# Kernel tuning notes

Measured on AMD Instinct MI355X. Metric: run time of the kernel, lower is better.

Reference implementation:

```python
import jax, jax.numpy as jnp
import numpy as np

B, LQ, LK = 4, 4096, 4096
D = 1024          # num_heads * key_dim = 16 * 64
Q_DIM = 1024      # query_dim
K_DIM = 1024      # note: linear_k input dim; here inputs carry d_model features
V_DIM = 1024      # value_dim


def setup_inputs() -> dict:
    key = jax.random.key(0)
    ks = jax.random.split(key, 12)
    s_in = 1.0 / np.sqrt(Q_DIM)
    s_d = 1.0 / np.sqrt(D)
    return {
        "q": jax.random.normal(ks[0], (B, LQ, Q_DIM), jnp.float32),
        "k": jax.random.normal(ks[1], (B, LK, K_DIM), jnp.float32),
        "v": jax.random.normal(ks[2], (B, LK, V_DIM), jnp.float32),
        # Linear weights stored [in, out] so projection is x @ W + b
        "Wq": jax.random.normal(ks[3], (Q_DIM, D), jnp.float32) * s_in,
        "bq": jax.random.normal(ks[4], (D,), jnp.float32) * s_in,
        "Wk": jax.random.normal(ks[5], (K_DIM, D), jnp.float32) * s_in,
        "bk": jax.random.normal(ks[6], (D,), jnp.float32) * s_in,
        "Wv": jax.random.normal(ks[7], (V_DIM, D), jnp.float32) * s_in,
        "bv": jax.random.normal(ks[8], (D,), jnp.float32) * s_in,
        "Wo": jax.random.normal(ks[9], (D, V_DIM), jnp.float32) * s_d,
        "bo": jax.random.normal(ks[10], (V_DIM,), jnp.float32) * s_d,
    }


def reference(q, k, v, Wq, bq, Wk, bk, Wv, bv, Wo, bo):
    # Projections: [B, L, D]
    qp = jax.nn.softmax(q @ Wq + bq, axis=-1)   # softmax over feature dim
    kp = jax.nn.softmax(k @ Wk + bk, axis=-2)   # softmax over sequence dim
    vp = jax.nn.softmax(v @ Wv + bv, axis=-2)   # softmax over sequence dim
    # Dropout is identity in eval mode (module uses dropout_p at train only).
    scores = jnp.einsum("bqd,bkd->bqk", qp, kp)  # [B, LQ, LK]
    ctx = jnp.einsum("bqk,bkd->bqd", scores, vp)  # [B, LQ, D]
    return ctx @ Wo + bo                          # [B, LQ, V_DIM]
```

## Files before the change

kernel.cpp:

```cpp
#include <hip/hip_runtime.h>

typedef float f32x4 __attribute__((ext_vector_type(4)));
typedef long lx2 __attribute__((ext_vector_type(2)));

__device__ __forceinline__ float h2f(unsigned short h) {
  return (float)__builtin_bit_cast(_Float16, h);
}
__device__ __forceinline__ unsigned short f2h(float f) {
  return __builtin_bit_cast(unsigned short, (_Float16)f);
}

#if __has_builtin(__builtin_amdgcn_cvt_pk_fp8_f32)
#define HW_FP8 1
#else
#define HW_FP8 0
#endif

__device__ __forceinline__ unsigned char f2e4_sw(float f) {
  unsigned short h = __builtin_bit_cast(unsigned short, (_Float16)f);
  unsigned s = (h >> 8) & 0x80u;
  unsigned ae = h & 0x7FFFu;
  if (ae >= 0x5F00u) return (unsigned char)(s | 0x7Eu);
  if (ae >= 0x2400u) {
    unsigned t = ae - 0x2000u;
    t = (t + 0x3Fu + ((t >> 7) & 1u)) >> 7;
    return (unsigned char)(s | t);
  }
  float v = (float)__builtin_bit_cast(_Float16, (unsigned short)ae) * 512.0f;
  int n = (int)rintf(v);
  return (unsigned char)(s | (unsigned)n);
}

__device__ __forceinline__ unsigned pk4e4(float a, float b, float c, float d) {
#if HW_FP8
  int lo = __builtin_amdgcn_cvt_pk_fp8_f32(a, b, 0, false);
  return (unsigned)__builtin_amdgcn_cvt_pk_fp8_f32(c, d, lo, true);
#else
  return (unsigned)f2e4_sw(a) | ((unsigned)f2e4_sw(b) << 8) |
         ((unsigned)f2e4_sw(c) << 16) | ((unsigned)f2e4_sw(d) << 24);
#endif
}
__device__ __forceinline__ unsigned pk2e4(float a, float b) {
#if HW_FP8
  return (unsigned)__builtin_amdgcn_cvt_pk_fp8_f32(a, b, 0, false) & 0xFFFFu;
#else
  return (unsigned)f2e4_sw(a) | ((unsigned)f2e4_sw(b) << 8);
#endif
}

__device__ __forceinline__ void gload_lds16(const void* g, void* l) {
  __builtin_amdgcn_global_load_lds(
      (const __attribute__((address_space(1))) void*)g,
      (__attribute__((address_space(3))) void*)l, 16, 0, 0);
}

__global__ __launch_bounds__(512, 4) void proj3(
    const float* __restrict__ A0, const float* __restrict__ A1,
    const float* __restrict__ A2, const unsigned char* __restrict__ WT8b,
    const float* __restrict__ b0, const float* __restrict__ b1,
    const float* __restrict__ b2, unsigned char* __restrict__ C0,
    unsigned char* __restrict__ C1, unsigned char* __restrict__ C2,
    float* __restrict__ s0, float* __restrict__ s1, float* __restrict__ s2)
{
  __shared__ alignas(16) unsigned char smem[49152];
  const int tid  = threadIdx.x;
  const int lane = tid & 63;
  const int wave = tid >> 6;
  const int waveM = wave >> 2;
  const int waveN = wave & 3;

  const int wg = (int)blockIdx.x;
  const int w  = (wg & 7) * 192 + (wg >> 3);
  const int z  = w / 512;
  const int wl = w - z * 512;
  const int x  = wl & 3;
  const int rem = wl >> 2;
  const int y  = rem & 31;
  const int bz = rem >> 5;

  const float* Af = (z == 0) ? A0 : (z == 1) ? A1 : A2;
  const float* bi = (z == 0) ? b0 : (z == 1) ? b1 : b2;
  unsigned char* Cp = (z == 0) ? C0 : (z == 1) ? C1 : C2;
  float* sums = (z == 0) ? s0 : (z == 1) ? s1 : s2;

  const int m0 = y * 128, n0 = x * 256;

  const int srow = tid >> 3;
  const int scol = ((tid * 16) & 127) ^ ((srow & 7) << 4);
  const unsigned char* BpR = WT8b + ((size_t)z << 20)
                             + (size_t)(n0 + srow) * 1024 + scol;
  const float* ApR = Af + (size_t)bz * (4096L * 1024)
                     + (size_t)(m0 + srow) * 1024 + scol;
  const unsigned oA0 = (unsigned)tid * 16;

  int offA[4], offB[4];
  {
    const int q16 = (lane >> 4) << 4;
#pragma unroll
    for (int mi = 0; mi < 4; ++mi) {
      const int r = waveM * 64 + mi * 16 + (lane & 15);
      offA[mi] = r * 128 + (q16 ^ ((r & 7) << 4));
    }
#pragma unroll
    for (int ni = 0; ni < 4; ++ni) {
      const int r = waveN * 64 + ni * 16 + (lane & 15);
      offB[ni] = 16384 + r * 128 + (q16 ^ ((r & 7) << 4));
    }
  }

  f32x4 acc[4][4] = {};

  float4 pa[4], pb[4];
#pragma unroll
  for (int j = 0; j < 4; ++j) {
    pa[j] = *(const float4*)(ApR + j * 4);
    pb[j] = *(const float4*)(ApR + 64 * 1024 + j * 4);
  }

  for (int kt = 0; kt < 8; ++kt) {
    {
      unsigned ua[4], ub[4];
#pragma unroll
      for (int j = 0; j < 4; ++j) {
        ua[j] = pk4e4(pa[j].x, pa[j].y, pa[j].z, pa[j].w);
        ub[j] = pk4e4(pb[j].x, pb[j].y, pb[j].z, pb[j].w);
      }
      *(uint4*)&smem[oA0]        = *(const uint4*)ua;
      *(uint4*)&smem[oA0 + 8192] = *(const uint4*)ub;
      if (kt + 1 < 8) {
        const float* s = ApR + (size_t)(kt + 1) * 128;
#pragma unroll
        for (int j = 0; j < 4; ++j) {
          pa[j] = *(const float4*)(s + j * 4);
          pb[j] = *(const float4*)(s + 64 * 1024 + j * 4);
        }
      }
    }
    const size_t kb = (size_t)kt * 128;
    gload_lds16(BpR + kb,              smem + 16384 + oA0);
    gload_lds16(BpR + 64 * 1024 + kb,  smem + 16384 + oA0 + 8192);
    gload_lds16(BpR + 128 * 1024 + kb, smem + 16384 + oA0 + 16384);
    gload_lds16(BpR + 192 * 1024 + kb, smem + 16384 + oA0 + 24576);
    __syncthreads();
#pragma unroll
    for (int kk = 0; kk < 2; ++kk) {
      const int kx = kk << 6;
      lx2 aF[4], bF[4];
#pragma unroll
      for (int mi = 0; mi < 4; ++mi) aF[mi] = *(const lx2*)&smem[offA[mi] ^ kx];
#pragma unroll
      for (int ni = 0; ni < 4; ++ni) bF[ni] = *(const lx2*)&smem[offB[ni] ^ kx];
#pragma unroll
      for (int h = 0; h < 2; ++h)
#pragma unroll
        for (int mi = 0; mi < 4; ++mi)
#pragma unroll
          for (int ni = 0; ni < 4; ++ni)
            acc[mi][ni] = __builtin_amdgcn_mfma_f32_16x16x32_fp8_fp8(
                aF[mi][h], bF[ni][h], acc[mi][ni], 0, 0, 0);
    }
    __syncthreads();
  }

  const int rb = (lane >> 4) * 4;
  const int cb_ = lane & 15;
  const long sC = 4096L * 1024;

  if (z == 0) {
#pragma unroll
    for (int m = 0; m < 4; ++m) {
      const int row0 = m0 + waveM * 64 + m * 16 + rb;
      float rs0 = 0, rs1 = 0, rs2 = 0, rs3 = 0;
#pragma unroll
      for (int n = 0; n < 4; ++n) {
        const int col = n0 + waveN * 64 + n * 16 + cb_;
        const float badd = bi[col];
        const float e0 = __expf(acc[m][n][0] * 0.125f + badd);
        const float e1 = __expf(acc[m][n][1] * 0.125f + badd);
        const float e2 = __expf(acc[m][n][2] * 0.125f + badd);
        const float e3 = __expf(acc[m][n][3] * 0.125f + badd);
        const unsigned p01 = pk2e4(e0 * 0.0625f, e1 * 0.0625f);
        const unsigned p23 = pk2e4(e2 * 0.0625f, e3 * 0.0625f);
        unsigned char* C8 = Cp + (long)bz * sC;
        C8[(size_t)(row0 + 0) * 1024 + col] = (unsigned char)(p01 & 0xff);
        C8[(size_t)(row0 + 1) * 1024 + col] = (unsigned char)((p01 >> 8) & 0xff);
        C8[(size_t)(row0 + 2) * 1024 + col] = (unsigned char)(p23 & 0xff);
        C8[(size_t)(row0 + 3) * 1024 + col] = (unsigned char)((p23 >> 8) & 0xff);
        rs0 += e0; rs1 += e1; rs2 += e2; rs3 += e3;
      }
#pragma unroll
      for (int off = 1; off <= 8; off <<= 1) {
        rs0 += __shfl_xor(rs0, off);
        rs1 += __shfl_xor(rs1, off);
        rs2 += __shfl_xor(rs2, off);
        rs3 += __shfl_xor(rs3, off);
      }
      if ((lane & 15) == 0) {
        float* s = sums + (size_t)bz * 4096 + row0;
        atomicAdd(s + 0, rs0);
        atomicAdd(s + 1, rs1);
        atomicAdd(s + 2, rs2);
        atomicAdd(s + 3, rs3);
      }
    }
  } else {
    float cs[4] = {0.f, 0.f, 0.f, 0.f};
#pragma unroll
    for (int m = 0; m < 4; ++m) {
      const int row0 = m0 + waveM * 64 + m * 16 + rb;
#pragma unroll
      for (int n = 0; n < 4; ++n) {
        const int col = n0 + waveN * 64 + n * 16 + cb_;
        const float badd = bi[col];
        float ev[4];
        float ls = 0.f;
#pragma unroll
        for (int r = 0; r < 4; ++r) {
          ev[r] = __expf(acc[m][n][r] * 0.125f + badd);
          ls += ev[r];
        }
        cs[n] += ls;
        *(unsigned*)(Cp + (long)bz * sC + ((size_t)col << 12) + row0) =
            pk4e4(ev[0] * 0.0625f, ev[1] * 0.0625f, ev[2] * 0.0625f, ev[3] * 0.0625f);
      }
    }
#pragma unroll
    for (int n = 0; n < 4; ++n) {
      cs[n] += __shfl_xor(cs[n], 16);
      cs[n] += __shfl_xor(cs[n], 32);
    }
    if (lane < 16) {
#pragma unroll
      for (int n = 0; n < 4; ++n) {
        const int col = n0 + waveN * 64 + n * 16 + lane;
        atomicAdd(sums + ((size_t)bz << 10) + col, cs[n]);
      }
    }
  }
}

template <int OUTMODE>
__global__ __launch_bounds__(512, 4) void gemm8(
    const unsigned char* __restrict__ A, const unsigned char* __restrict__ Bt,
    void* __restrict__ Cv, const float* __restrict__ bias,
    const float* __restrict__ sums,
    int N, int K, int ldk, int gx, int gy, int nsplit,
    long sA, long sB, long sC)
{
  __shared__ alignas(16) unsigned char smem[49152];
  const int tid  = threadIdx.x;
  const int lane = tid & 63;
  const int wave = tid >> 6;
  const int waveM = wave >> 2;
  const int waveN = wave & 3;

  const int nwg = (int)gridDim.x;
  const int cpx = nwg >> 3;
  const int wg  = (int)blockIdx.x;
  const int w   = (wg & 7) * cpx + (wg >> 3);
  const int x   = w % gx;
  const int rem = w / gx;
  const int y   = rem % gy;
  const int zt  = rem / gy;
  const int bz  = zt / nsplit;
  const int sp  = zt % nsplit;

  const int m0 = y * 128, n0 = x * 256;
  const size_t ldkB = (size_t)ldk;
  const size_t ldkB64 = ldkB * 64, ldkB128 = ldkB * 128;

  const int srow = tid >> 3;
  const int scol = ((tid * 16) & 127) ^ ((srow & 7) << 4);
  const char* ApR;
  const char* BpR;
  {
    const char* Ab = (const char*)A + (long)bz * sA + (long)sp * K + (size_t)m0 * ldkB;
    const char* Bb = (const char*)Bt + (long)bz * sB + (long)sp * K + (size_t)n0 * ldkB;
    ApR = Ab + (size_t)srow * ldkB + scol;
    BpR = Bb + (size_t)srow * ldkB + scol;
  }
  const unsigned oA0 = (unsigned)tid * 16;

  int offA[4], offB[4];
  {
    const int q16 = (lane >> 4) << 4;
#pragma unroll
    for (int mi = 0; mi < 4; ++mi) {
      const int r = waveM * 64 + mi * 16 + (lane & 15);
      offA[mi] = r * 128 + (q16 ^ ((r & 7) << 4));
    }
#pragma unroll
    for (int ni = 0; ni < 4; ++ni) {
      const int r = waveN * 64 + ni * 16 + (lane & 15);
      offB[ni] = 16384 + r * 128 + (q16 ^ ((r & 7) << 4));
    }
  }

  f32x4 acc[4][4] = {};

  const int nk = K >> 7;
  for (int kt = 0; kt < nk; ++kt) {
    const size_t kb = (size_t)kt * 128;
    gload_lds16(ApR + kb,                     smem + oA0);
    gload_lds16(ApR + ldkB64 + kb,            smem + oA0 + 8192);
    gload_lds16(BpR + kb,                     smem + 16384 + oA0);
    gload_lds16(BpR + ldkB64 + kb,            smem + 16384 + oA0 + 8192);
    gload_lds16(BpR + ldkB128 + kb,           smem + 16384 + oA0 + 16384);
    gload_lds16(BpR + ldkB128 + ldkB64 + kb,  smem + 16384 + oA0 + 24576);
    __syncthreads();
#pragma unroll
    for (int kk = 0; kk < 2; ++kk) {
      const int kx = kk << 6;
      lx2 aF[4], bF[4];
#pragma unroll
      for (int mi = 0; mi < 4; ++mi) aF[mi] = *(const lx2*)&smem[offA[mi] ^ kx];
#pragma unroll
      for (int ni = 0; ni < 4; ++ni) bF[ni] = *(const lx2*)&smem[offB[ni] ^ kx];
#pragma unroll
      for (int h = 0; h < 2; ++h)
#pragma unroll
        for (int mi = 0; mi < 4; ++mi)
#pragma unroll
          for (int ni = 0; ni < 4; ++ni)
            acc[mi][ni] = __builtin_amdgcn_mfma_f32_16x16x32_fp8_fp8(
                aF[mi][h], bF[ni][h], acc[mi][ni], 0, 0, 0);
    }
    __syncthreads();
  }

  const int rb = (lane >> 4) * 4;
  const int cb_ = lane & 15;
  const long zout = (OUTMODE == 2) ? (long)zt : (long)bz;
#pragma unroll
  for (int m = 0; m < 4; ++m) {
    const int row0 = m0 + waveM * 64 + m * 16 + rb;
    float i0 = 0, i1 = 0, i2 = 0, i3 = 0;
    if (OUTMODE == 5) {
      const float4 s4 = *(const float4*)&sums[(size_t)zout * 4096 + row0];
      i0 = 1.0f / (256.0f * s4.x); i1 = 1.0f / (256.0f * s4.y);
      i2 = 1.0f / (256.0f * s4.z); i3 = 1.0f / (256.0f * s4.w);
    }
#pragma unroll
    for (int n = 0; n < 4; ++n) {
      const int col = n0 + waveN * 64 + n * 16 + cb_;
      if (OUTMODE == 2) {
#pragma unroll
        for (int r = 0; r < 4; ++r)
          ((unsigned short*)Cv)[zout * sC + (size_t)(row0 + r) * N + col] = f2h(acc[m][n][r]);
      } else {
        const float badd = bias[col];
        float* C32 = (float*)Cv;
        C32[zout * sC + (size_t)(row0 + 0) * N + col] = acc[m][n][0] * i0 + badd;
        C32[zout * sC + (size_t)(row0 + 1) * N + col] = acc[m][n][1] * i1 + badd;
        C32[zout * sC + (size_t)(row0 + 2) * N + col] = acc[m][n][2] * i2 + badd;
        C32[zout * sC + (size_t)(row0 + 3) * N + col] = acc[m][n][3] * i3 + badd;
      }
    }
  }
}

__global__ __launch_bounds__(256) void w_tr8(
    const float* __restrict__ W0, const float* __restrict__ W1,
    const float* __restrict__ W2, const float* __restrict__ W3,
    unsigned char* __restrict__ WT8b)
{
  __shared__ float tile[64][65];
  const int z = blockIdx.z;
  const float* W = (z == 0) ? W0 : (z == 1) ? W1 : (z == 2) ? W2 : W3;
  unsigned char* WT8 = WT8b + ((size_t)z << 20);
  const int c0 = blockIdx.x * 64;
  const int r0 = blockIdx.y * 64;
  const int tid = threadIdx.x;
  const int r = tid >> 2;
  const int cq = (tid & 3) * 16;
#pragma unroll
  for (int i = 0; i < 4; ++i) {
    const int c = cq + i * 4;
    const float4 v = *(const float4*)&W[(size_t)(r0 + r) * 1024 + c0 + c];
    tile[r][c + 0] = v.x;
    tile[r][c + 1] = v.y;
    tile[r][c + 2] = v.z;
    tile[r][c + 3] = v.w;
  }
  __syncthreads();
  const int c = tid >> 2;
  const int rq = (tid & 3) * 16;
  unsigned u4[4];
#pragma unroll
  for (int j = 0; j < 4; ++j)
    u4[j] = pk4e4(tile[rq + 4 * j + 0][c] * 8.f, tile[rq + 4 * j + 1][c] * 8.f,
                  tile[rq + 4 * j + 2][c] * 8.f, tile[rq + 4 * j + 3][c] * 8.f);
  *(uint4*)(WT8 + (size_t)(c0 + c) * 1024 + r0 + rq) = *(const uint4*)u4;
}

__global__ __launch_bounds__(256) void red4m(
    const unsigned short* __restrict__ P, const float* __restrict__ skr,
    const float* __restrict__ svr, unsigned char* __restrict__ O)
{
  const int i = blockIdx.x * 256 + threadIdx.x;
  const int b = i >> 18;
  const int j = i & 262143;
  const int dk = j >> 8;
  const int dv0 = (j & 255) << 2;
  float s0 = 0, s1 = 0, s2 = 0, s3 = 0;
#pragma unroll
  for (int sl = 0; sl < 4; ++sl) {
    const uint2 u = *(const uint2*)(P + (((long)(b * 4 + sl)) << 20) + ((long)j << 2));
    s0 += h2f(u.x & 0xffff); s1 += h2f(u.x >> 16);
    s2 += h2f(u.y & 0xffff); s3 += h2f(u.y >> 16);
  }
  const float fk = 4194304.0f / skr[(b << 10) + dk];
  const float4 fv = *(const float4*)&svr[(b << 10) + dv0];
  ((unsigned*)O)[i] = pk4e4(s0 * fk / fv.x, s1 * fk / fv.y,
                            s2 * fk / fv.z, s3 * fk / fv.w);
}

__global__ __launch_bounds__(256) void red4g(
    const unsigned short* __restrict__ P, unsigned char* __restrict__ O)
{
  const int i = blockIdx.x * 256 + threadIdx.x;
  const int b = i >> 18;
  const int j = i & 262143;
  float s0 = 0, s1 = 0, s2 = 0, s3 = 0;
#pragma unroll
  for (int sl = 0; sl < 4; ++sl) {
    const uint2 u = *(const uint2*)(P + (((long)(b * 4 + sl)) << 20) + ((long)j << 2));
    s0 += h2f(u.x & 0xffff); s1 += h2f(u.x >> 16);
    s2 += h2f(u.y & 0xffff); s3 += h2f(u.y >> 16);
  }
  ((unsigned*)O)[i] = pk4e4(s0 * 0.03125f, s1 * 0.03125f,
                            s2 * 0.03125f, s3 * 0.03125f);
}

extern "C" void kernel_launch(void* const* d_in, const int* in_sizes, int n_in,
                              void* d_out, int out_size, void* d_ws, size_t ws_size,
                              hipStream_t stream) {
  const float* q  = (const float*)d_in[0];
  const float* k  = (const float*)d_in[1];
  const float* v  = (const float*)d_in[2];
  const float* Wq = (const float*)d_in[3];
  const float* bq = (const float*)d_in[4];
  const float* Wk = (const float*)d_in[5];
  const float* bk = (const float*)d_in[6];
  const float* Wv = (const float*)d_in[7];
  const float* bv = (const float*)d_in[8];
  const float* Wo = (const float*)d_in[9];
  const float* bo = (const float*)d_in[10];
  float* out = (float*)d_out;

  char* p = (char*)d_ws;
  unsigned short* Part = (unsigned short*)p; p += 33554432;
  unsigned char* WT8b = (unsigned char*)p;   p += 4194304;
  unsigned char* Eq8  = (unsigned char*)p;   p += 16777216;
  unsigned char* ETk8 = (unsigned char*)p;   p += 16777216;
  unsigned char* ETv8 = (unsigned char*)p;   p += 16777216;
  unsigned char* Mh8  = (unsigned char*)p;   p += 4194304;
  unsigned char* GT8  = (unsigned char*)p;   p += 4194304;
  float* sqraw = (float*)p; p += 16384 * 4;
  float* skraw = (float*)p; p += 4096 * 4;
  float* svraw = (float*)p; p += 4096 * 4;

  const dim3 blk(256);
  const dim3 blk512(512);
  const long S22 = 4096L * 1024;
  const long S20 = 1024L * 1024;

  hipMemsetAsync(sqraw, 0, (16384 + 4096 + 4096) * sizeof(float), stream);

  w_tr8<<<dim3(16, 16, 4), blk, 0, stream>>>(Wq, Wk, Wv, Wo, WT8b);

  proj3<<<1536, blk512, 0, stream>>>(q, k, v, WT8b, bq, bk, bv,
                                     Eq8, ETk8, ETv8, sqraw, skraw, svraw);

  gemm8<2><<<512, blk512, 0, stream>>>(ETk8, ETv8, Part, nullptr, nullptr,
      1024, 1024, 4096, 4, 8, 4, S22, S22, S20);
  red4m<<<4096, blk, 0, stream>>>(Part, skraw, svraw, Mh8);

  gemm8<2><<<512, blk512, 0, stream>>>(WT8b + (3L << 20), Mh8, Part, nullptr, nullptr,
      1024, 256, 1024, 4, 8, 4, 0, S20, S20);
  red4g<<<4096, blk, 0, stream>>>(Part, GT8);

  gemm8<5><<<512, blk512, 0, stream>>>(Eq8, GT8, out, bo, sqraw,
      1024, 1024, 1024, 4, 32, 1, S22, S20, S22);

  (void)in_sizes; (void)n_in; (void)out_size; (void)ws_size;
}
```

Measured before the change: 280.8 us.

## Pre-convert fp32 activations to fp8 in a separate pass before projection GEMM

Adds a conv3 kernel that converts the q, k and v fp32 activations to packed fp8 in one streaming pass into new workspace buffers. The proj3 GEMM then loads its A tiles with direct global-to-LDS 16-byte loads, the same way it already loads the weights. This removes the in-loop fp32 loads, register conversion and manual LDS stores, and cuts the A-tile traffic that the four N-tile blocks re-read. In exchange it adds a kernel launch, an extra write and read of 48MB of fp8 data, and 48MB more workspace.

```diff
diff --git a/kernel.cpp b/kernel.cpp
--- a/kernel.cpp
+++ b/kernel.cpp
@@ -54,9 +54,26 @@
       (__attribute__((address_space(3))) void*)l, 16, 0, 0);
 }
 
+__global__ __launch_bounds__(256) void conv3(
+    const float* __restrict__ A0, const float* __restrict__ A1,
+    const float* __restrict__ A2, unsigned char* __restrict__ X0,
+    unsigned char* __restrict__ X1, unsigned char* __restrict__ X2)
+{
+  const int z = blockIdx.y;
+  const float* in = (z == 0) ? A0 : (z == 1) ? A1 : A2;
+  unsigned char* out = (z == 0) ? X0 : (z == 1) ? X1 : X2;
+  const size_t i = (size_t)blockIdx.x * 256 + threadIdx.x;
+  const float4 a = ((const float4*)in)[i * 2];
+  const float4 b = ((const float4*)in)[i * 2 + 1];
+  uint2 o;
+  o.x = pk4e4(a.x, a.y, a.z, a.w);
+  o.y = pk4e4(b.x, b.y, b.z, b.w);
+  ((uint2*)out)[i] = o;
+}
+
 __global__ __launch_bounds__(512, 4) void proj3(
-    const float* __restrict__ A0, const float* __restrict__ A1,
-    const float* __restrict__ A2, const unsigned char* __restrict__ WT8b,
+    const unsigned char* __restrict__ X0, const unsigned char* __restrict__ X1,
+    const unsigned char* __restrict__ X2, const unsigned char* __restrict__ WT8b,
     const float* __restrict__ b0, const float* __restrict__ b1,
     const float* __restrict__ b2, unsigned char* __restrict__ C0,
     unsigned char* __restrict__ C1, unsigned char* __restrict__ C2,
@@ -78,7 +95,7 @@
   const int y  = rem & 31;
   const int bz = rem >> 5;
 
-  const float* Af = (z == 0) ? A0 : (z == 1) ? A1 : A2;
+  const unsigned char* Xf = (z == 0) ? X0 : (z == 1) ? X1 : X2;
   const float* bi = (z == 0) ? b0 : (z == 1) ? b1 : b2;
   unsigned char* Cp = (z == 0) ? C0 : (z == 1) ? C1 : C2;
   float* sums = (z == 0) ? s0 : (z == 1) ? s1 : s2;
@@ -89,8 +106,8 @@
   const int scol = ((tid * 16) & 127) ^ ((srow & 7) << 4);
   const unsigned char* BpR = WT8b + ((size_t)z << 20)
                              + (size_t)(n0 + srow) * 1024 + scol;
-  const float* ApR = Af + (size_t)bz * (4096L * 1024)
-                     + (size_t)(m0 + srow) * 1024 + scol;
+  const unsigned char* ApR = Xf + (size_t)bz * (4096L * 1024)
+                             + (size_t)(m0 + srow) * 1024 + scol;
   const unsigned oA0 = (unsigned)tid * 16;
 
   int offA[4], offB[4];
@@ -110,33 +127,10 @@
 
   f32x4 acc[4][4] = {};
 
-  float4 pa[4], pb[4];
-#pragma unroll
-  for (int j = 0; j < 4; ++j) {
-    pa[j] = *(const float4*)(ApR + j * 4);
-    pb[j] = *(const float4*)(ApR + 64 * 1024 + j * 4);
-  }
-
   for (int kt = 0; kt < 8; ++kt) {
-    {
-      unsigned ua[4], ub[4];
-#pragma unroll
-      for (int j = 0; j < 4; ++j) {
-        ua[j] = pk4e4(pa[j].x, pa[j].y, pa[j].z, pa[j].w);
-        ub[j] = pk4e4(pb[j].x, pb[j].y, pb[j].z, pb[j].w);
-      }
-      *(uint4*)&smem[oA0]        = *(const uint4*)ua;
-      *(uint4*)&smem[oA0 + 8192] = *(const uint4*)ub;
-      if (kt + 1 < 8) {
-        const float* s = ApR + (size_t)(kt + 1) * 128;
-#pragma unroll
-        for (int j = 0; j < 4; ++j) {
-          pa[j] = *(const float4*)(s + j * 4);
-          pb[j] = *(const float4*)(s + 64 * 1024 + j * 4);
-        }
-      }
-    }
     const size_t kb = (size_t)kt * 128;
+    gload_lds16(ApR + kb,              smem + oA0);
+    gload_lds16(ApR + 64 * 1024 + kb,  smem + oA0 + 8192);
     gload_lds16(BpR + kb,              smem + 16384 + oA0);
     gload_lds16(BpR + 64 * 1024 + kb,  smem + 16384 + oA0 + 8192);
     gload_lds16(BpR + 128 * 1024 + kb, smem + 16384 + oA0 + 16384);
@@ -451,6 +445,9 @@
   char* p = (char*)d_ws;
   unsigned short* Part = (unsigned short*)p; p += 33554432;
   unsigned char* WT8b = (unsigned char*)p;   p += 4194304;
+  unsigned char* Xq8  = (unsigned char*)p;   p += 16777216;
+  unsigned char* Xk8  = (unsigned char*)p;   p += 16777216;
+  unsigned char* Xv8  = (unsigned char*)p;   p += 16777216;
   unsigned char* Eq8  = (unsigned char*)p;   p += 16777216;
   unsigned char* ETk8 = (unsigned char*)p;   p += 16777216;
   unsigned char* ETv8 = (unsigned char*)p;   p += 16777216;
@@ -469,7 +466,9 @@
 
   w_tr8<<<dim3(16, 16, 4), blk, 0, stream>>>(Wq, Wk, Wv, Wo, WT8b);
 
-  proj3<<<1536, blk512, 0, stream>>>(q, k, v, WT8b, bq, bk, bv,
+  conv3<<<dim3(8192, 3), blk, 0, stream>>>(q, k, v, Xq8, Xk8, Xv8);
+
+  proj3<<<1536, blk512, 0, stream>>>(Xq8, Xk8, Xv8, WT8b, bq, bk, bv,
                                      Eq8, ETk8, ETv8, sqraw, skraw, svraw);
 
   gemm8<2><<<512, blk512, 0, stream>>>(ETk8, ETv8, Part, nullptr, nullptr,
```

After: 230.1 us (median of 2 runs). 1.22x faster.
